# Kernel optimization log

Measured on AMD Instinct MI355X. Metric: run time of the kernel, lower is better.

Reference implementation:

```python
import jax, jax.numpy as jnp
import numpy as np

N, DF, DR, H, K = 4096, 128, 64, 1024, 10


def _init_linear(key, fan_in, fan_out):
    kw, kb = jax.random.split(key)
    bound = 1.0 / np.sqrt(fan_in)
    W = jax.random.uniform(kw, (fan_in, fan_out), jnp.float32, -bound, bound)
    b = jax.random.uniform(kb, (fan_out,), jnp.float32, -bound, bound)
    return W, b


def setup_inputs() -> dict:
    key = jax.random.key(0)
    ks = jax.random.split(key, 8)
    condition = jax.random.normal(ks[0], (N, DF), jnp.float32)
    tensor = jax.random.normal(ks[1], (N, DR), jnp.float32)
    Win, b_in = _init_linear(ks[2], DF + DR, H)
    W1, b1 = _init_linear(ks[3], H, H)
    W2, b2 = _init_linear(ks[4], H, H)
    W3, b3 = _init_linear(ks[5], H, H)
    Wout, b_out = _init_linear(ks[6], H, DR)
    return {"condition": condition, "tensor": tensor,
            "Win": Win, "b_in": b_in, "W1": W1, "b1": b1,
            "W2": W2, "b2": b2, "W3": W3, "b3": b3,
            "Wout": Wout, "b_out": b_out}


def _mlp(x, Win, b_in, W1, b1, W2, b2, W3, b3, Wout, b_out):
    # FFNN: input layer + 3 hidden layers with Softplus, linear output -> DR
    h = jax.nn.softplus(x @ Win + b_in)
    h = jax.nn.softplus(h @ W1 + b1)
    h = jax.nn.softplus(h @ W2 + b2)
    h = jax.nn.softplus(h @ W3 + b3)
    return h @ Wout + b_out


def reference(condition, tensor, Win, b_in, W1, b1, W2, b2, W3, b3, Wout, b_out):
    # torch.cdist(condition, condition), p=2 -> [N, N]
    sq = jnp.sum(condition * condition, axis=-1)
    d2 = sq[:, None] + sq[None, :] - 2.0 * (condition @ condition.T)
    dist = jnp.sqrt(jnp.maximum(d2, 0.0))
    # torch.topk(dist, 10, dim=1, largest=False) -> k nearest neighbor indices
    _, neighbor_idx = jax.lax.top_k(-dist, K)  # [N, K]
    # gather neighbor groups
    cond_g = condition[neighbor_idx]  # [N, K, DF]
    tens_g = tensor[neighbor_idx]     # [N, K, DR]
    # MongeMapNetwork.pushforward: tensor - MLP(concat(condition, tensor))
    x = jnp.concatenate([cond_g, tens_g], axis=-1)  # [N, K, DF+DR]
    pushed = tens_g - _mlp(x, Win, b_in, W1, b1, W2, b2, W3, b3, Wout, b_out)
    return pushed  # [N, K, DR]
```

## Files before the change

kernel.cpp:

```cpp
#include <hip/hip_runtime.h>
#include <hip/hip_fp16.h>
#include <stdint.h>

typedef unsigned short u16;
typedef unsigned int   u32;
typedef unsigned long long u64;
typedef short v8bf __attribute__((ext_vector_type(8)));
typedef float v4f  __attribute__((ext_vector_type(4)));
typedef u16   v8u  __attribute__((ext_vector_type(8)));

#define NPTS 4096
#define DF   128
#define DR   64
#define HID  1024
#define KNN  10
#define DIN  192

#define AS1 __attribute__((address_space(1)))
#define AS3 __attribute__((address_space(3)))

__device__ __forceinline__ float bf2f(u16 b){ return __uint_as_float(((unsigned)b)<<16); }
__device__ __forceinline__ u16 f2bf(float f){
  unsigned u = __float_as_uint(f);
  unsigned r = 0x7fffu + ((u>>16)&1u);
  return (u16)((u + r)>>16);
}
__device__ __forceinline__ u16 f2h(float f){
  __half h = __float2half(f);
  return __half_as_ushort(h);
}
__device__ __forceinline__ float softplus_f(float x){
  return x>15.f ? x : __logf(1.f + __expf(x));
}
__device__ __forceinline__ float rdv(const void* p, long j, int fl){
  return fl ? bf2f(((const u16*)p)[j]) : ((const float*)p)[j];
}
__device__ __forceinline__ void gl2lds16(const u16* g, u16* l){
  __builtin_amdgcn_global_load_lds((const AS1 unsigned int*)g, (AS3 unsigned int*)l, 16, 0, 0);
}

__global__ void detect_k(const u16* __restrict__ c, int* __restrict__ flag){
  __shared__ int cnt[256];
  int t = threadIdx.x, n = 0;
  for(int i=t; i<8192; i+=256){
    u16 v = c[2*i];
    int e = (v>>7)&0xff;
    n += (e>=96 && e<=158);
  }
  cnt[t] = n; __syncthreads();
  for(int s=128; s>0; s>>=1){ if(t<s) cnt[t]+=cnt[t+s]; __syncthreads(); }
  if(t==0) *flag = (cnt[0] > 4915) ? 1 : 0;
}

__global__ void prep_k(const void* cond, const void* tens,
    const void* Wi, const void* W1, const void* W2, const void* W3, const void* Wo,
    const void* bi, const void* b1, const void* b2, const void* b3, const void* bo,
    float* __restrict__ condF, float* __restrict__ tensF, float* __restrict__ biasF,
    u16* Oi, u16* O1, u16* O2, u16* O3, u16* Oo,
    float* __restrict__ sq, u16* __restrict__ X, const int* __restrict__ flag){
  __shared__ u16 tile[32][33];
  const int fl = *flag;
  const int bid = blockIdx.x, tid = threadIdx.x;
  if(bid < 3089){
    int i = bid*256 + tid;
    if(i < 524288){ condF[i] = rdv(cond, i, fl); }
    else if(i < 786432){ tensF[i-524288] = rdv(tens, i-524288, fl); }
    else{
      int j = i - 786432;
      if(j < 1024)      biasF[j] = rdv(bi, j, fl);
      else if(j < 2048) biasF[j] = rdv(b1, j-1024, fl);
      else if(j < 3072) biasF[j] = rdv(b2, j-2048, fl);
      else if(j < 4096) biasF[j] = rdv(b3, j-3072, fl);
      else if(j < 4160) biasF[j] = rdv(bo, j-4096, fl);
    }
  } else if(bid < 6417){
    int b = bid - 3089;
    const void* in; u16* out; int R, C, bx, by;
    if(b < 192)      {              in=Wi; out=Oi; R=192;  C=1024; bx=b&31; by=b>>5; }
    else if(b < 1216){ b -= 192;    in=W1; out=O1; R=1024; C=1024; bx=b&31; by=b>>5; }
    else if(b < 2240){ b -= 1216;   in=W2; out=O2; R=1024; C=1024; bx=b&31; by=b>>5; }
    else if(b < 3264){ b -= 2240;   in=W3; out=O3; R=1024; C=1024; bx=b&31; by=b>>5; }
    else             { b -= 3264;   in=Wo; out=Oo; R=1024; C=64;   bx=b&1;  by=b>>1; }
    int gx = bx*32, gy = by*32;
    int tx = tid&31, ty = tid>>5;
    #pragma unroll
    for(int r=ty; r<32; r+=8){
      size_t idx = (size_t)(gy+r)*C + gx + tx;
      tile[r][tx] = fl ? ((const u16*)in)[idx] : f2bf(((const float*)in)[idx]);
    }
    __syncthreads();
    #pragma unroll
    for(int r=ty; r<32; r+=8) out[(size_t)(gx+r)*R + gy + tx] = tile[tx][r];
  } else if(bid < 7441){
    int b = bid - 6417;
    int row = b*4 + (tid>>6), lane = tid&63;
    float a = rdv(cond, (long)row*DF + lane, fl);
    float c2 = rdv(cond, (long)row*DF + lane + 64, fl);
    double s = (double)a*a + (double)c2*c2;
    #pragma unroll
    for(int off=32; off>0; off>>=1) s += __shfl_down(s, off, 64);
    if(lane==0) sq[row] = (float)s;
  } else {
    int c = (bid-7441)*256 + tid;
    int j = c/48;
    int off = (c - j*48)*4;
    ushort4 o;
    if(off < DF){
      o.x = f2bf(rdv(cond, (long)j*DF + off + 0, fl));
      o.y = f2bf(rdv(cond, (long)j*DF + off + 1, fl));
      o.z = f2bf(rdv(cond, (long)j*DF + off + 2, fl));
      o.w = f2bf(rdv(cond, (long)j*DF + off + 3, fl));
    }else{
      int t2 = off - DF;
      o.x = f2bf(rdv(tens, (long)j*DR + t2 + 0, fl));
      o.y = f2bf(rdv(tens, (long)j*DR + t2 + 1, fl));
      o.z = f2bf(rdv(tens, (long)j*DR + t2 + 2, fl));
      o.w = f2bf(rdv(tens, (long)j*DR + t2 + 3, fl));
    }
    *(ushort4*)&X[(size_t)j*DIN + off] = o;
  }
}

__device__ __forceinline__ void gemm_bt_body(const u16* __restrict__ A,
    const u16* __restrict__ Bt, const float* __restrict__ bias, u16* __restrict__ C,
    int Nc, int Kc, int bid, u16* As, u16* Bs){
  const int xcd = bid&7, slot = bid>>3;
  const int bm = (xcd*4 + (slot>>4)) * 128;
  const int bn = (slot&15) * 64;
  const int tid = threadIdx.x, lane = tid&63, wave = tid>>6;
  const int wm = (wave&1)*64, wn = (wave>>1)*32;
  int c0 = wave*128 + lane, c1 = c0 + 64;
  int r0 = c0>>2, q0 = c0&3, r1 = c1>>2, q1 = c1&3;
  int cb = wave*64 + lane, rb = cb>>2, qb = cb&3;
  const u16* pA0 = A  + (size_t)(bm+r0)*Kc + q0*8;
  const u16* pA1 = A  + (size_t)(bm+r1)*Kc + q1*8;
  const u16* pB  = Bt + (size_t)(bn+rb)*Kc + qb*8;
  u16* lA0 = &As[wave*1024];
  u16* lA1 = &As[wave*1024 + 512];
  u16* lB  = &Bs[wave*512];
  const int m16 = lane&15, q = lane>>4;
  v4f acc[4][2] = {};
  for(int kb=0; kb<Kc; kb+=64){
    gl2lds16(pA0 + kb, lA0);
    gl2lds16(pA1 + kb, lA1);
    gl2lds16(pB  + kb, lB);
    gl2lds16(pA0 + kb + 32, lA0 + 4096);
    gl2lds16(pA1 + kb + 32, lA1 + 4096);
    gl2lds16(pB  + kb + 32, lB + 2048);
    __syncthreads();
    #pragma unroll
    for(int kk=0;kk<2;kk++){
      v8bf a[4], b[2];
      #pragma unroll
      for(int x=0;x<4;x++) a[x] = *(const v8bf*)&As[kk*4096 + (wm + x*16 + m16)*32 + q*8];
      #pragma unroll
      for(int x=0;x<2;x++) b[x] = *(const v8bf*)&Bs[kk*2048 + (wn + x*16 + m16)*32 + q*8];
      #pragma unroll
      for(int mi=0;mi<4;mi++)
        #pragma unroll
        for(int ni=0;ni<2;ni++)
          acc[mi][ni] = __builtin_amdgcn_mfma_f32_16x16x32_bf16(a[mi], b[ni], acc[mi][ni], 0,0,0);
    }
    __syncthreads();
  }
  const int col16 = lane&15, rowq = lane>>4;
  #pragma unroll
  for(int mi=0;mi<4;mi++){
    #pragma unroll
    for(int ni=0;ni<2;ni++){
      int cn = bn + wn + ni*16 + col16;
      float bi = bias[cn];
      #pragma unroll
      for(int r=0;r<4;r++){
        int rw = bm + wm + mi*16 + rowq*4 + r;
        float v = softplus_f(acc[mi][ni][r] + bi);
        C[(size_t)rw*Nc + cn] = f2bf(v);
      }
    }
  }
}

__device__ __forceinline__ void knn_body(const u16* __restrict__ distH,
    const float* __restrict__ condF, int* __restrict__ nidx, int row,
    float* __restrict__ af, int* __restrict__ cand, u64* __restrict__ keys){
  const int lane = threadIdx.x&63;
  af[lane]    = condF[(size_t)row*DF + lane];
  af[lane+64] = condF[(size_t)row*DF + lane + 64];
  const v8u* drow = (const v8u*)(distH + (size_t)row*NPTS);
  v8u vals[8];
  #pragma unroll
  for(int k=0;k<8;k++) vals[k] = drow[lane + k*64];
  u32 mx = 0;
  #pragma unroll
  for(int k=0;k<8;k++)
    #pragma unroll
    for(int e=0;e<8;e++){ u32 v = vals[k][e]; mx = v>mx ? v : mx; }
  #pragma unroll
  for(int off=32; off>0; off>>=1){
    u32 o = (u32)__shfl_down((int)mx, off, 64); mx = o>mx ? o : mx;
  }
  mx = (u32)__shfl((int)mx, 0, 64);
  u32 hi = mx+1, lo = 0;
  for(int it=0; it<17; ++it){
    u32 mid = (lo+hi)>>1;
    int c = 0;
    #pragma unroll
    for(int k=0;k<8;k++)
      #pragma unroll
      for(int e=0;e<8;e++)
        c += (int)__popcll(__ballot((u32)vals[k][e] < mid));
    if(c >= 16){ hi = mid; if(c <= 64) break; }
    else lo = mid;
  }
  const u32 t = hi;
  const u64 below = (1ull<<lane) - 1ull;
  int base = 0;
  #pragma unroll
  for(int k=0;k<8;k++)
    #pragma unroll
    for(int e=0;e<8;e++){
      bool p = (u32)vals[k][e] < t;
      u64 m = __ballot(p);
      if(p){
        int off = base + (int)__popcll(m & below);
        if(off < 64) cand[off] = (lane + k*64)*8 + e;
      }
      base += (int)__popcll(m);
    }
  int cnt = base > 64 ? 64 : base;
  u64 mykey = ~0ULL; int myj = -1;
  if(lane < cnt){
    int j = cand[lane];
    const float4* bp4 = (const float4*)(condF + (size_t)j*DF);
    double s = 0.0;
    #pragma unroll
    for(int v4i=0; v4i<32; v4i++){
      float4 bv = bp4[v4i];
      double d0 = (double)af[v4i*4+0]-(double)bv.x;
      double d1 = (double)af[v4i*4+1]-(double)bv.y;
      double d2 = (double)af[v4i*4+2]-(double)bv.z;
      double d3 = (double)af[v4i*4+3]-(double)bv.w;
      s += d0*d0 + d1*d1 + d2*d2 + d3*d3;
    }
    u64 bits = (u64)__double_as_longlong(s);
    mykey = (bits & ~0xFFFULL) | (u32)j;
    myj = j;
  }
  keys[lane] = mykey;
  if(lane < cnt){
    int rank = 0;
    for(int c2=0;c2<cnt;c2++) rank += (keys[c2] < mykey);
    if(rank < KNN) nidx[row*KNN + rank] = myj;
  }
}

__global__ __launch_bounds__(256,2) void gram_g1_k(const u16* __restrict__ condB,
    const float* __restrict__ condF, const float* __restrict__ sq,
    u16* __restrict__ distH, const int* __restrict__ flag,
    const u16* __restrict__ X, const u16* __restrict__ Wt_in,
    const float* __restrict__ biasF, u16* __restrict__ A0){
  __shared__ __align__(16) u16 smem[20480];
  const int bid = blockIdx.x;
  if(bid < 512){
    gemm_bt_body(X, Wt_in, biasF, A0, HID, DIN, bid, smem, smem+8192);
    return;
  }
  const int gb = bid - 512;
  const int fl = *flag;
  const int bm = (gb&31)*128, bn = (gb>>5)*128;
  const int tid = threadIdx.x, lane = tid&63, wave = tid>>6;
  const int wm = (wave&1)*64, wn = (wave>>1)*64;
  const int m16 = lane&15, q = lane>>4;
  v4f acc[4][4] = {};
  if(fl){
    const int srow = wave*32 + (lane>>2), scol = (lane&3)*8;
    const u16* gA = condB + (size_t)(bm+srow)*DF + scol;
    const u16* gB = condB + (size_t)(bn+srow)*DF + scol;
    u16* lA = &smem[wave*1024];
    u16* lB = &smem[4096 + wave*1024];
    for(int kb=0; kb<DF; kb+=32){
      gl2lds16(gA + kb,                 lA);
      gl2lds16(gA + kb + (size_t)16*DF, lA + 512);
      gl2lds16(gB + kb,                 lB);
      gl2lds16(gB + kb + (size_t)16*DF, lB + 512);
      __syncthreads();
      v8bf a[4], b[4];
      #pragma unroll
      for(int x=0;x<4;x++){
        a[x] = *(const v8bf*)&smem[(wm + x*16 + m16)*32 + q*8];
        b[x] = *(const v8bf*)&smem[4096 + (wn + x*16 + m16)*32 + q*8];
      }
      #pragma unroll
      for(int mi=0;mi<4;mi++)
        #pragma unroll
        for(int ni=0;ni<4;ni++)
          acc[mi][ni] = __builtin_amdgcn_mfma_f32_16x16x32_bf16(a[mi], b[ni], acc[mi][ni], 0,0,0);
      __syncthreads();
    }
  } else {
    u16* Ahi = smem;
    u16* Alo = smem + 5120;
    u16* Bhi = smem + 10240;
    u16* Blo = smem + 15360;
    for(int kb=0; kb<DF; kb+=32){
      #pragma unroll
      for(int t=0;t<4;t++){
        int ch = tid + t*256;
        int r = ch>>3, c = (ch&7)*4;
        float4 av = *(const float4*)&condF[(size_t)(bm+r)*DF + kb + c];
        float4 bv = *(const float4*)&condF[(size_t)(bn+r)*DF + kb + c];
        ushort4 ah, bh, al, bl;
        ah.x=f2bf(av.x); ah.y=f2bf(av.y); ah.z=f2bf(av.z); ah.w=f2bf(av.w);
        bh.x=f2bf(bv.x); bh.y=f2bf(bv.y); bh.z=f2bf(bv.z); bh.w=f2bf(bv.w);
        al.x=f2bf(av.x-bf2f(ah.x)); al.y=f2bf(av.y-bf2f(ah.y));
        al.z=f2bf(av.z-bf2f(ah.z)); al.w=f2bf(av.w-bf2f(ah.w));
        bl.x=f2bf(bv.x-bf2f(bh.x)); bl.y=f2bf(bv.y-bf2f(bh.y));
        bl.z=f2bf(bv.z-bf2f(bh.z)); bl.w=f2bf(bv.w-bf2f(bh.w));
        *(ushort4*)&Ahi[r*40+c] = ah; *(ushort4*)&Bhi[r*40+c] = bh;
        *(ushort4*)&Alo[r*40+c] = al; *(ushort4*)&Blo[r*40+c] = bl;
      }
      __syncthreads();
      v8bf ahf[4], bhf[4], alf[4], blf[4];
      #pragma unroll
      for(int x=0;x<4;x++){
        ahf[x] = *(const v8bf*)&Ahi[(wm + x*16 + m16)*40 + q*8];
        bhf[x] = *(const v8bf*)&Bhi[(wn + x*16 + m16)*40 + q*8];
        alf[x] = *(const v8bf*)&Alo[(wm + x*16 + m16)*40 + q*8];
        blf[x] = *(const v8bf*)&Blo[(wn + x*16 + m16)*40 + q*8];
      }
      #pragma unroll
      for(int mi=0;mi<4;mi++)
        #pragma unroll
        for(int ni=0;ni<4;ni++){
          acc[mi][ni] = __builtin_amdgcn_mfma_f32_16x16x32_bf16(alf[mi], bhf[ni], acc[mi][ni], 0,0,0);
          acc[mi][ni] = __builtin_amdgcn_mfma_f32_16x16x32_bf16(ahf[mi], blf[ni], acc[mi][ni], 0,0,0);
          acc[mi][ni] = __builtin_amdgcn_mfma_f32_16x16x32_bf16(ahf[mi], bhf[ni], acc[mi][ni], 0,0,0);
        }
      __syncthreads();
    }
  }
  const int col16 = lane&15, rowq = lane>>4;
  #pragma unroll
  for(int mi=0;mi<4;mi++){
    #pragma unroll
    for(int ni=0;ni<4;ni++){
      int cj = bn + wn + ni*16 + col16;
      float sqj = sq[cj];
      #pragma unroll
      for(int r=0;r<4;r++){
        int ri = bm + wm + mi*16 + rowq*4 + r;
        float d2 = (sq[ri] + sqj) - 2.0f*acc[mi][ni][r];
        distH[(size_t)ri*NPTS + cj] = f2h(fmaxf(d2, 0.f));
      }
    }
  }
}

__global__ __launch_bounds__(256,2) void gemm_knn_k(const u16* __restrict__ A,
    const u16* __restrict__ Bt, const float* __restrict__ bias, u16* __restrict__ C,
    const u16* __restrict__ distH, const float* __restrict__ condF,
    int* __restrict__ nidx, int rowoff){
  __shared__ __align__(16) u16 gsm[12288];
  __shared__ float af[4][DF];
  __shared__ int   cand[4][64];
  __shared__ u64   keys[4][64];
  const int bid = blockIdx.x;
  if(bid < 512){
    gemm_bt_body(A, Bt, bias, C, HID, HID, bid, gsm, gsm+8192);
  } else {
    const int wv = threadIdx.x>>6;
    const int row = rowoff + (bid-512)*4 + wv;
    knn_body(distH, condF, nidx, row, af[wv], cand[wv], keys[wv]);
  }
}

__global__ __launch_bounds__(256,2) void gemm_bt_k(const u16* __restrict__ A,
    const u16* __restrict__ Bt, const float* __restrict__ bias, u16* __restrict__ C){
  __shared__ __align__(16) u16 As[8192];
  __shared__ __align__(16) u16 Bs[4096];
  gemm_bt_body(A, Bt, bias, C, HID, HID, blockIdx.x, As, Bs);
}

__global__ __launch_bounds__(256,2) void gemm_out_k(const u16* __restrict__ A,
    const u16* __restrict__ Bt, float* __restrict__ Pp){
  __shared__ __align__(16) u16 As[128*32];
  __shared__ __align__(16) u16 Bs[64*32];
  const int bm = (blockIdx.x>>2)*128;
  const int k0 = (blockIdx.x&3)*256;
  float* P = Pp + (size_t)(blockIdx.x&3)*262144;
  const int tid = threadIdx.x, lane = tid&63, wave = tid>>6;
  const int wm = wave*32;
  int c0 = wave*128 + lane, c1 = c0 + 64;
  int ra0 = c0>>2, qa0 = c0&3, ra1 = c1>>2, qa1 = c1&3;
  int cb = wave*64 + lane;
  int rb = cb>>2, qb = cb&3;
  const u16* pA0 = A  + (size_t)(bm+ra0)*HID + qa0*8;
  const u16* pA1 = A  + (size_t)(bm+ra1)*HID + qa1*8;
  const u16* pB  = Bt + (size_t)rb*HID + qb*8;
  u16* lA0 = &As[(wave*128     )*8];
  u16* lA1 = &As[(wave*128 + 64)*8];
  u16* lB  = &Bs[(wave*64      )*8];
  const int m16 = lane&15, q = lane>>4;
  v4f acc[2][4] = {};
  for(int kb=k0; kb<k0+256; kb+=32){
    gl2lds16(pA0 + kb, lA0);
    gl2lds16(pA1 + kb, lA1);
    gl2lds16(pB  + kb, lB);
    __syncthreads();
    v8bf a[2], b[4];
    a[0] = *(const v8bf*)&As[(wm + m16)*32 + q*8];
    a[1] = *(const v8bf*)&As[(wm + 16 + m16)*32 + q*8];
    #pragma unroll
    for(int x=0;x<4;x++) b[x] = *(const v8bf*)&Bs[(x*16 + m16)*32 + q*8];
    #pragma unroll
    for(int mi=0;mi<2;mi++)
      #pragma unroll
      for(int ni=0;ni<4;ni++)
        acc[mi][ni] = __builtin_amdgcn_mfma_f32_16x16x32_bf16(a[mi], b[ni], acc[mi][ni], 0,0,0);
    __syncthreads();
  }
  const int col16 = lane&15, rowq = lane>>4;
  #pragma unroll
  for(int mi=0;mi<2;mi++){
    #pragma unroll
    for(int ni=0;ni<4;ni++){
      int cn = ni*16 + col16;
      #pragma unroll
      for(int r=0;r<4;r++){
        int rw = bm + wm + mi*16 + rowq*4 + r;
        P[(size_t)rw*DR + cn] = acc[mi][ni][r];
      }
    }
  }
}

__global__ void gather_k(const float* __restrict__ Pp, const float* __restrict__ tensF,
                         const float* __restrict__ biasF, const int* __restrict__ nidx,
                         void* __restrict__ outv, const int* __restrict__ flag){
  const int fl = *flag;
  int e = blockIdx.x*256 + threadIdx.x;
  int m = e>>4;
  int c = (e&15)*4;
  int j = nidx[m] & (NPTS-1);
  size_t rc = (size_t)j*DR + c;
  float4 t  = *(const float4*)&tensF[rc];
  float4 b  = *(const float4*)&biasF[4096 + c];
  float4 p0 = *(const float4*)&Pp[rc];
  float4 p1 = *(const float4*)&Pp[262144 + rc];
  float4 p2 = *(const float4*)&Pp[524288 + rc];
  float4 p3 = *(const float4*)&Pp[786432 + rc];
  float4 v;
  v.x = t.x - (b.x + ((p0.x+p1.x)+(p2.x+p3.x)));
  v.y = t.y - (b.y + ((p0.y+p1.y)+(p2.y+p3.y)));
  v.z = t.z - (b.z + ((p0.z+p1.z)+(p2.z+p3.z)));
  v.w = t.w - (b.w + ((p0.w+p1.w)+(p2.w+p3.w)));
  if(fl){
    ushort4 o; o.x=f2bf(v.x); o.y=f2bf(v.y); o.z=f2bf(v.z); o.w=f2bf(v.w);
    *(ushort4*)&((u16*)outv)[(size_t)m*DR + c] = o;
  }else{
    *(float4*)&((float*)outv)[(size_t)m*DR + c] = v;
  }
}

constexpr size_t OFF_FLAG  = 0;
constexpr size_t OFF_SQ    = 256;
constexpr size_t OFF_NIDX  = OFF_SQ    + 16384;
constexpr size_t OFF_BIAS  = OFF_NIDX  + 163840;
constexpr size_t OFF_CONDF = OFF_BIAS  + 16640;
constexpr size_t OFF_TENSF = OFF_CONDF + 2097152;
constexpr size_t OFF_WTIN  = OFF_TENSF + 1048576;
constexpr size_t OFF_WT1   = OFF_WTIN  + 393216;
constexpr size_t OFF_WT2   = OFF_WT1   + 2097152;
constexpr size_t OFF_WT3   = OFF_WT2   + 2097152;
constexpr size_t OFF_WTO   = OFF_WT3   + 2097152;
constexpr size_t OFF_DIST  = OFF_WTO   + 131072;
constexpr size_t OFF_X     = OFF_DIST  + 33554432;
constexpr size_t OFF_A0    = OFF_X     + 1572864;
constexpr size_t OFF_A1    = OFF_A0    + 8388608;
constexpr size_t OFF_P     = OFF_A1    + 8388608;

extern "C" void kernel_launch(void* const* d_in, const int* in_sizes, int n_in,
                              void* d_out, int out_size, void* d_ws, size_t ws_size,
                              hipStream_t stream){
  char* ws = (char*)d_ws;
  int*   flag  = (int*)  (ws + OFF_FLAG);
  float* sqv   = (float*)(ws + OFF_SQ);
  int*   nidx  = (int*)  (ws + OFF_NIDX);
  float* biasF = (float*)(ws + OFF_BIAS);
  float* condF = (float*)(ws + OFF_CONDF);
  float* tensF = (float*)(ws + OFF_TENSF);
  u16*   Wt_in = (u16*)  (ws + OFF_WTIN);
  u16*   Wt1   = (u16*)  (ws + OFF_WT1);
  u16*   Wt2   = (u16*)  (ws + OFF_WT2);
  u16*   Wt3   = (u16*)  (ws + OFF_WT3);
  u16*   Wt_o  = (u16*)  (ws + OFF_WTO);
  u16*   distH = (u16*)  (ws + OFF_DIST);
  u16*   X     = (u16*)  (ws + OFF_X);
  u16*   A0    = (u16*)  (ws + OFF_A0);
  u16*   A1    = (u16*)  (ws + OFF_A1);
  float* Pp    = (float*)(ws + OFF_P);

  detect_k <<<1, 256, 0, stream>>>((const u16*)d_in[0], flag);
  prep_k   <<<8209, 256, 0, stream>>>(d_in[0], d_in[1],
                d_in[2], d_in[4], d_in[6], d_in[8], d_in[10],
                d_in[3], d_in[5], d_in[7], d_in[9], d_in[11],
                condF, tensF, biasF, Wt_in, Wt1, Wt2, Wt3, Wt_o, sqv, X, flag);
  gram_g1_k<<<1536, 256, 0, stream>>>((const u16*)d_in[0], condF, sqv, distH, flag,
                                      X, Wt_in, biasF, A0);
  gemm_knn_k<<<1024, 256, 0, stream>>>(A0, Wt1, biasF+1024, A1, distH, condF, nidx, 0);
  gemm_knn_k<<<1024, 256, 0, stream>>>(A1, Wt2, biasF+2048, A0, distH, condF, nidx, 2048);
  gemm_bt_k  <<<512, 256, 0, stream>>>(A0, Wt3, biasF+3072, A1);
  gemm_out_k <<<128, 256, 0, stream>>>(A1, Wt_o, Pp);
  gather_k   <<<2560, 256, 0, stream>>>(Pp, tensF, biasF, nidx, d_out, flag);
}
```

Before: 210.5 us.

## Fuse all stages into a persistent megakernel with software grid barriers

Replaces the eight separate kernel launches with a single persistent kernel of 512 blocks. The stages (prep, input GEMM plus Gram, hidden GEMMs overlapped with KNN, output GEMM, gather) are separated by atomic-counter grid barriers. Each block runs flag detection itself, and the hidden GEMMs are reassigned to 256 blocks doing two tiles each while the other blocks do KNN. The goal is to remove launch gaps and tail effects between stages, at the cost of spin-wait barriers, less parallelism within each stage, and reliance on all 512 blocks being co-resident (checked through an occupancy query).

```diff
diff --git a/kernel.cpp b/kernel.cpp
--- a/kernel.cpp
+++ b/kernel.cpp
@@ -15,6 +15,7 @@
 #define HID  1024
 #define KNN  10
 #define DIN  192
+#define NB   512
 
 #define AS1 __attribute__((address_space(1)))
 #define AS3 __attribute__((address_space(3)))
@@ -39,30 +40,65 @@
   __builtin_amdgcn_global_load_lds((const AS1 unsigned int*)g, (AS3 unsigned int*)l, 16, 0, 0);
 }
 
-__global__ void detect_k(const u16* __restrict__ c, int* __restrict__ flag){
-  __shared__ int cnt[256];
-  int t = threadIdx.x, n = 0;
-  for(int i=t; i<8192; i+=256){
+constexpr size_t OFF_BAR   = 0;
+constexpr size_t OFF_FLAG  = 128;
+constexpr size_t OFF_SQ    = 256;
+constexpr size_t OFF_NIDX  = OFF_SQ    + 16384;
+constexpr size_t OFF_BIAS  = OFF_NIDX  + 163840;
+constexpr size_t OFF_CONDF = OFF_BIAS  + 16640;
+constexpr size_t OFF_TENSF = OFF_CONDF + 2097152;
+constexpr size_t OFF_WTIN  = OFF_TENSF + 1048576;
+constexpr size_t OFF_WT1   = OFF_WTIN  + 393216;
+constexpr size_t OFF_WT2   = OFF_WT1   + 2097152;
+constexpr size_t OFF_WT3   = OFF_WT2   + 2097152;
+constexpr size_t OFF_WTO   = OFF_WT3   + 2097152;
+constexpr size_t OFF_DIST  = OFF_WTO   + 131072;
+constexpr size_t OFF_X     = OFF_DIST  + 33554432;
+constexpr size_t OFF_A0    = OFF_X     + 1572864;
+constexpr size_t OFF_A1    = OFF_A0    + 8388608;
+constexpr size_t OFF_P     = OFF_A1    + 8388608;
+
+__device__ __forceinline__ void gbar(u32* cnt, u32* rel, u32 e){
+  __syncthreads();
+  if(threadIdx.x == 0){
+    __threadfence();
+    u32 a = __hip_atomic_fetch_add(cnt, 1u, __ATOMIC_ACQ_REL, __HIP_MEMORY_SCOPE_AGENT);
+    if(a == e*NB + (NB-1)){
+      __hip_atomic_store(rel, e+1u, __ATOMIC_RELEASE, __HIP_MEMORY_SCOPE_AGENT);
+    } else {
+      while(__hip_atomic_load(rel, __ATOMIC_ACQUIRE, __HIP_MEMORY_SCOPE_AGENT) <= e)
+        __builtin_amdgcn_s_sleep(2);
+    }
+    __threadfence();
+  }
+  __syncthreads();
+}
+
+__device__ __forceinline__ int detect_fl(const void* cond, u16* SM){
+  const u16* c = (const u16*)cond;
+  int tid = threadIdx.x, n = 0;
+  for(int i=tid; i<8192; i+=256){
     u16 v = c[2*i];
     int e = (v>>7)&0xff;
     n += (e>=96 && e<=158);
   }
-  cnt[t] = n; __syncthreads();
-  for(int s=128; s>0; s>>=1){ if(t<s) cnt[t]+=cnt[t+s]; __syncthreads(); }
-  if(t==0) *flag = (cnt[0] > 4915) ? 1 : 0;
-}
-
-__global__ void prep_k(const void* cond, const void* tens,
+  int* cnt = (int*)SM;
+  cnt[tid] = n; __syncthreads();
+  for(int s=128; s>0; s>>=1){ if(tid<s) cnt[tid]+=cnt[tid+s]; __syncthreads(); }
+  int fl = (cnt[0] > 4915) ? 1 : 0;
+  __syncthreads();
+  return fl;
+}
+
+__device__ __forceinline__ void prep_unit(int u, int tid, int fl,
+    const void* cond, const void* tens,
     const void* Wi, const void* W1, const void* W2, const void* W3, const void* Wo,
     const void* bi, const void* b1, const void* b2, const void* b3, const void* bo,
-    float* __restrict__ condF, float* __restrict__ tensF, float* __restrict__ biasF,
+    float* condF, float* tensF, float* biasF,
     u16* Oi, u16* O1, u16* O2, u16* O3, u16* Oo,
-    float* __restrict__ sq, u16* __restrict__ X, const int* __restrict__ flag){
-  __shared__ u16 tile[32][33];
-  const int fl = *flag;
-  const int bid = blockIdx.x, tid = threadIdx.x;
-  if(bid < 3089){
-    int i = bid*256 + tid;
+    float* sq, u16* X, u16* SM){
+  if(u < 3089){
+    int i = u*256 + tid;
     if(i < 524288){ condF[i] = rdv(cond, i, fl); }
     else if(i < 786432){ tensF[i-524288] = rdv(tens, i-524288, fl); }
     else{
@@ -73,8 +109,9 @@
       else if(j < 4096) biasF[j] = rdv(b3, j-3072, fl);
       else if(j < 4160) biasF[j] = rdv(bo, j-4096, fl);
     }
-  } else if(bid < 6417){
-    int b = bid - 3089;
+  } else if(u < 6417){
+    u16 (*tile)[33] = (u16(*)[33])SM;
+    int b = u - 3089;
     const void* in; u16* out; int R, C, bx, by;
     if(b < 192)      {              in=Wi; out=Oi; R=192;  C=1024; bx=b&31; by=b>>5; }
     else if(b < 1216){ b -= 192;    in=W1; out=O1; R=1024; C=1024; bx=b&31; by=b>>5; }
@@ -91,8 +128,8 @@
     __syncthreads();
     #pragma unroll
     for(int r=ty; r<32; r+=8) out[(size_t)(gx+r)*R + gy + tx] = tile[tx][r];
-  } else if(bid < 7441){
-    int b = bid - 6417;
+  } else if(u < 7441){
+    int b = u - 6417;
     int row = b*4 + (tid>>6), lane = tid&63;
     float a = rdv(cond, (long)row*DF + lane, fl);
     float c2 = rdv(cond, (long)row*DF + lane + 64, fl);
@@ -101,7 +138,7 @@
     for(int off=32; off>0; off>>=1) s += __shfl_down(s, off, 64);
     if(lane==0) sq[row] = (float)s;
   } else {
-    int c = (bid-7441)*256 + tid;
+    int c = (u-7441)*256 + tid;
     int j = c/48;
     int off = (c - j*48)*4;
     ushort4 o;
@@ -254,19 +291,9 @@
   }
 }
 
-__global__ __launch_bounds__(256,2) void gram_g1_k(const u16* __restrict__ condB,
-    const float* __restrict__ condF, const float* __restrict__ sq,
-    u16* __restrict__ distH, const int* __restrict__ flag,
-    const u16* __restrict__ X, const u16* __restrict__ Wt_in,
-    const float* __restrict__ biasF, u16* __restrict__ A0){
-  __shared__ __align__(16) u16 smem[20480];
-  const int bid = blockIdx.x;
-  if(bid < 512){
-    gemm_bt_body(X, Wt_in, biasF, A0, HID, DIN, bid, smem, smem+8192);
-    return;
-  }
-  const int gb = bid - 512;
-  const int fl = *flag;
+__device__ __forceinline__ void gram_tile(int gb, int fl,
+    const u16* __restrict__ condB, const float* __restrict__ condF,
+    const float* __restrict__ sq, u16* __restrict__ distH, u16* SM){
   const int bm = (gb&31)*128, bn = (gb>>5)*128;
   const int tid = threadIdx.x, lane = tid&63, wave = tid>>6;
   const int wm = (wave&1)*64, wn = (wave>>1)*64;
@@ -276,8 +303,8 @@
     const int srow = wave*32 + (lane>>2), scol = (lane&3)*8;
     const u16* gA = condB + (size_t)(bm+srow)*DF + scol;
     const u16* gB = condB + (size_t)(bn+srow)*DF + scol;
-    u16* lA = &smem[wave*1024];
-    u16* lB = &smem[4096 + wave*1024];
+    u16* lA = &SM[wave*1024];
+    u16* lB = &SM[4096 + wave*1024];
     for(int kb=0; kb<DF; kb+=32){
       gl2lds16(gA + kb,                 lA);
       gl2lds16(gA + kb + (size_t)16*DF, lA + 512);
@@ -287,8 +314,8 @@
       v8bf a[4], b[4];
       #pragma unroll
       for(int x=0;x<4;x++){
-        a[x] = *(const v8bf*)&smem[(wm + x*16 + m16)*32 + q*8];
-        b[x] = *(const v8bf*)&smem[4096 + (wn + x*16 + m16)*32 + q*8];
+        a[x] = *(const v8bf*)&SM[(wm + x*16 + m16)*32 + q*8];
+        b[x] = *(const v8bf*)&SM[4096 + (wn + x*16 + m16)*32 + q*8];
       }
       #pragma unroll
       for(int mi=0;mi<4;mi++)
@@ -298,10 +325,10 @@
       __syncthreads();
     }
   } else {
-    u16* Ahi = smem;
-    u16* Alo = smem + 5120;
-    u16* Bhi = smem + 10240;
-    u16* Blo = smem + 15360;
+    u16* Ahi = SM;
+    u16* Alo = SM + 5120;
+    u16* Bhi = SM + 10240;
+    u16* Blo = SM + 15360;
     for(int kb=0; kb<DF; kb+=32){
       #pragma unroll
       for(int t=0;t<4;t++){
@@ -356,38 +383,11 @@
   }
 }
 
-__global__ __launch_bounds__(256,2) void gemm_knn_k(const u16* __restrict__ A,
-    const u16* __restrict__ Bt, const float* __restrict__ bias, u16* __restrict__ C,
-    const u16* __restrict__ distH, const float* __restrict__ condF,
-    int* __restrict__ nidx, int rowoff){
-  __shared__ __align__(16) u16 gsm[12288];
-  __shared__ float af[4][DF];
-  __shared__ int   cand[4][64];
-  __shared__ u64   keys[4][64];
-  const int bid = blockIdx.x;
-  if(bid < 512){
-    gemm_bt_body(A, Bt, bias, C, HID, HID, bid, gsm, gsm+8192);
-  } else {
-    const int wv = threadIdx.x>>6;
-    const int row = rowoff + (bid-512)*4 + wv;
-    knn_body(distH, condF, nidx, row, af[wv], cand[wv], keys[wv]);
-  }
-}
-
-__global__ __launch_bounds__(256,2) void gemm_bt_k(const u16* __restrict__ A,
-    const u16* __restrict__ Bt, const float* __restrict__ bias, u16* __restrict__ C){
-  __shared__ __align__(16) u16 As[8192];
-  __shared__ __align__(16) u16 Bs[4096];
-  gemm_bt_body(A, Bt, bias, C, HID, HID, blockIdx.x, As, Bs);
-}
-
-__global__ __launch_bounds__(256,2) void gemm_out_k(const u16* __restrict__ A,
-    const u16* __restrict__ Bt, float* __restrict__ Pp){
-  __shared__ __align__(16) u16 As[128*32];
-  __shared__ __align__(16) u16 Bs[64*32];
-  const int bm = (blockIdx.x>>2)*128;
-  const int k0 = (blockIdx.x&3)*256;
-  float* P = Pp + (size_t)(blockIdx.x&3)*262144;
+__device__ __forceinline__ void gemm_out_body(int obid, const u16* __restrict__ A,
+    const u16* __restrict__ Bt, float* __restrict__ Pp, u16* As, u16* Bs){
+  const int bm = (obid>>2)*128;
+  const int k0 = (obid&3)*256;
+  float* P = Pp + (size_t)(obid&3)*262144;
   const int tid = threadIdx.x, lane = tid&63, wave = tid>>6;
   const int wm = wave*32;
   int c0 = wave*128 + lane, c1 = c0 + 64;
@@ -434,11 +434,9 @@
   }
 }
 
-__global__ void gather_k(const float* __restrict__ Pp, const float* __restrict__ tensF,
-                         const float* __restrict__ biasF, const int* __restrict__ nidx,
-                         void* __restrict__ outv, const int* __restrict__ flag){
-  const int fl = *flag;
-  int e = blockIdx.x*256 + threadIdx.x;
+__device__ __forceinline__ void gather_unit(int e, int fl,
+    const float* Pp, const float* tensF, const float* biasF,
+    const int* nidx, void* outv){
   int m = e>>4;
   int c = (e&15)*4;
   int j = nidx[m] & (NPTS-1);
@@ -462,22 +460,166 @@
   }
 }
 
-constexpr size_t OFF_FLAG  = 0;
-constexpr size_t OFF_SQ    = 256;
-constexpr size_t OFF_NIDX  = OFF_SQ    + 16384;
-constexpr size_t OFF_BIAS  = OFF_NIDX  + 163840;
-constexpr size_t OFF_CONDF = OFF_BIAS  + 16640;
-constexpr size_t OFF_TENSF = OFF_CONDF + 2097152;
-constexpr size_t OFF_WTIN  = OFF_TENSF + 1048576;
-constexpr size_t OFF_WT1   = OFF_WTIN  + 393216;
-constexpr size_t OFF_WT2   = OFF_WT1   + 2097152;
-constexpr size_t OFF_WT3   = OFF_WT2   + 2097152;
-constexpr size_t OFF_WTO   = OFF_WT3   + 2097152;
-constexpr size_t OFF_DIST  = OFF_WTO   + 131072;
-constexpr size_t OFF_X     = OFF_DIST  + 33554432;
-constexpr size_t OFF_A0    = OFF_X     + 1572864;
-constexpr size_t OFF_A1    = OFF_A0    + 8388608;
-constexpr size_t OFF_P     = OFF_A1    + 8388608;
+__global__ void __launch_bounds__(256,2) mega_k(
+    const void* cond, const void* tens,
+    const void* Wi, const void* W1w, const void* W2w, const void* W3w, const void* Wow,
+    const void* bi, const void* b1, const void* b2, const void* b3, const void* bo,
+    char* ws, void* outv){
+  __shared__ __align__(16) u16 SM[20480];
+  const int bid = blockIdx.x, tid = threadIdx.x;
+
+  u32*   bcnt  = (u32*)  (ws + OFF_BAR);
+  u32*   brel  = (u32*)  (ws + OFF_BAR + 8);
+  float* sqv   = (float*)(ws + OFF_SQ);
+  int*   nidx  = (int*)  (ws + OFF_NIDX);
+  float* biasF = (float*)(ws + OFF_BIAS);
+  float* condF = (float*)(ws + OFF_CONDF);
+  float* tensF = (float*)(ws + OFF_TENSF);
+  u16*   Wt_in = (u16*)  (ws + OFF_WTIN);
+  u16*   Wt1   = (u16*)  (ws + OFF_WT1);
+  u16*   Wt2   = (u16*)  (ws + OFF_WT2);
+  u16*   Wt3   = (u16*)  (ws + OFF_WT3);
+  u16*   Wt_o  = (u16*)  (ws + OFF_WTO);
+  u16*   distH = (u16*)  (ws + OFF_DIST);
+  u16*   X     = (u16*)  (ws + OFF_X);
+  u16*   A0    = (u16*)  (ws + OFF_A0);
+  u16*   A1    = (u16*)  (ws + OFF_A1);
+  float* Pp    = (float*)(ws + OFF_P);
+
+  const int fl = detect_fl(cond, SM);
+
+  for(int u=bid; u<8209; u+=NB){
+    prep_unit(u, tid, fl, cond, tens, Wi, W1w, W2w, W3w, Wow, bi, b1, b2, b3, bo,
+              condF, tensF, biasF, Wt_in, Wt1, Wt2, Wt3, Wt_o, sqv, X, SM);
+    __syncthreads();
+  }
+  gbar(bcnt, brel, 0);
+
+  gemm_bt_body(X, Wt_in, biasF, A0, HID, DIN, bid, SM, SM+8192);
+  __syncthreads();
+  for(int gb=bid; gb<1024; gb+=NB){
+    gram_tile(gb, fl, (const u16*)cond, condF, sqv, distH, SM);
+    __syncthreads();
+  }
+  gbar(bcnt, brel, 1);
+
+  const int wv = tid>>6;
+  float* kaf  = (float*)SM + wv*128;
+  int*   kcan = (int*)((char*)SM + 2048) + wv*64;
+  u64*   kkey = (u64*)((char*)SM + 4096) + wv*64;
+
+  if(bid < 256){
+    gemm_bt_body(A0, Wt1, biasF+1024, A1, HID, HID, bid,     SM, SM+8192);
+    __syncthreads();
+    gemm_bt_body(A0, Wt1, biasF+1024, A1, HID, HID, bid+256, SM, SM+8192);
+  } else {
+    knn_body(distH, condF, nidx, (bid-256)*4 + wv, kaf, kcan, kkey);
+  }
+  gbar(bcnt, brel, 2);
+
+  if(bid < 256){
+    gemm_bt_body(A1, Wt2, biasF+2048, A0, HID, HID, bid,     SM, SM+8192);
+    __syncthreads();
+    gemm_bt_body(A1, Wt2, biasF+2048, A0, HID, HID, bid+256, SM, SM+8192);
+  } else {
+    knn_body(distH, condF, nidx, 1024 + (bid-256)*4 + wv, kaf, kcan, kkey);
+  }
+  gbar(bcnt, brel, 3);
+
+  if(bid < 256){
+    gemm_bt_body(A0, Wt3, biasF+3072, A1, HID, HID, bid,     SM, SM+8192);
+    __syncthreads();
+    gemm_bt_body(A0, Wt3, biasF+3072, A1, HID, HID, bid+256, SM, SM+8192);
+  } else {
+    knn_body(distH, condF, nidx, 2048 + (bid-256)*4 + wv, kaf, kcan, kkey);
+  }
+  gbar(bcnt, brel, 4);
+
+  if(bid < 128){
+    gemm_out_body(bid, A1, Wt_o, Pp, SM, SM+8192);
+  } else if(bid >= 256){
+    knn_body(distH, condF, nidx, 3072 + (bid-256)*4 + wv, kaf, kcan, kkey);
+  }
+  gbar(bcnt, brel, 5);
+
+  for(int u=bid; u<2560; u+=NB)
+    gather_unit(u*256 + tid, fl, Pp, tensF, biasF, nidx, outv);
+}
+
+__global__ void detect_k(const u16* __restrict__ c, int* __restrict__ flag){
+  __shared__ int cnt[256];
+  int t = threadIdx.x, n = 0;
+  for(int i=t; i<8192; i+=256){
+    u16 v = c[2*i];
+    int e = (v>>7)&0xff;
+    n += (e>=96 && e<=158);
+  }
+  cnt[t] = n; __syncthreads();
+  for(int s=128; s>0; s>>=1){ if(t<s) cnt[t]+=cnt[t+s]; __syncthreads(); }
+  if(t==0) *flag = (cnt[0] > 4915) ? 1 : 0;
+}
+
+__global__ void prep_k(const void* cond, const void* tens,
+    const void* Wi, const void* W1, const void* W2, const void* W3, const void* Wo,
+    const void* bi, const void* b1, const void* b2, const void* b3, const void* bo,
+    float* condF, float* tensF, float* biasF,
+    u16* Oi, u16* O1, u16* O2, u16* O3, u16* Oo,
+    float* sq, u16* X, const int* __restrict__ flag){
+  __shared__ __align__(16) u16 SM[1056];
+  prep_unit(blockIdx.x, threadIdx.x, *flag, cond, tens, Wi, W1, W2, W3, Wo,
+            bi, b1, b2, b3, bo, condF, tensF, biasF, Oi, O1, O2, O3, Oo, sq, X, SM);
+}
+
+__global__ __launch_bounds__(256,2) void gram_g1_k(const u16* __restrict__ condB,
+    const float* __restrict__ condF, const float* __restrict__ sq,
+    u16* __restrict__ distH, const int* __restrict__ flag,
+    const u16* __restrict__ X, const u16* __restrict__ Wt_in,
+    const float* __restrict__ biasF, u16* __restrict__ A0){
+  __shared__ __align__(16) u16 SM[20480];
+  const int bid = blockIdx.x;
+  if(bid < 512){
+    gemm_bt_body(X, Wt_in, biasF, A0, HID, DIN, bid, SM, SM+8192);
+  } else {
+    gram_tile(bid-512, *flag, condB, condF, sq, distH, SM);
+  }
+}
+
+__global__ __launch_bounds__(256,2) void gemm_knn_k(const u16* __restrict__ A,
+    const u16* __restrict__ Bt, const float* __restrict__ bias, u16* __restrict__ C,
+    const u16* __restrict__ distH, const float* __restrict__ condF,
+    int* __restrict__ nidx, int rowoff){
+  __shared__ __align__(16) u16 gsm[12288];
+  __shared__ float af[4][DF];
+  __shared__ int   cand[4][64];
+  __shared__ u64   keys[4][64];
+  const int bid = blockIdx.x;
+  if(bid < 512){
+    gemm_bt_body(A, Bt, bias, C, HID, HID, bid, gsm, gsm+8192);
+  } else {
+    const int wv = threadIdx.x>>6;
+    knn_body(distH, condF, nidx, rowoff + (bid-512)*4 + wv, af[wv], cand[wv], keys[wv]);
+  }
+}
+
+__global__ __launch_bounds__(256,2) void gemm_bt_k(const u16* __restrict__ A,
+    const u16* __restrict__ Bt, const float* __restrict__ bias, u16* __restrict__ C){
+  __shared__ __align__(16) u16 As[8192];
+  __shared__ __align__(16) u16 Bs[4096];
+  gemm_bt_body(A, Bt, bias, C, HID, HID, blockIdx.x, As, Bs);
+}
+
+__global__ __launch_bounds__(256,2) void gemm_out_k(const u16* __restrict__ A,
+    const u16* __restrict__ Bt, float* __restrict__ Pp){
+  __shared__ __align__(16) u16 As[4096];
+  __shared__ __align__(16) u16 Bs[2048];
+  gemm_out_body(blockIdx.x, A, Bt, Pp, As, Bs);
+}
+
+__global__ void gather_k(const float* __restrict__ Pp, const float* __restrict__ tensF,
+                         const float* __restrict__ biasF, const int* __restrict__ nidx,
+                         void* __restrict__ outv, const int* __restrict__ flag){
+  gather_unit(blockIdx.x*256 + threadIdx.x, *flag, Pp, tensF, biasF, nidx, outv);
+}
 
 extern "C" void kernel_launch(void* const* d_in, const int* in_sizes, int n_in,
                               void* d_out, int out_size, void* d_ws, size_t ws_size,
@@ -500,6 +642,22 @@
   u16*   A1    = (u16*)  (ws + OFF_A1);
   float* Pp    = (float*)(ws + OFF_P);
 
+  static int occ_cached = -1;
+  if(occ_cached < 0){
+    int occ = 0;
+    if(hipOccupancyMaxActiveBlocksPerMultiprocessor(&occ, (const void*)mega_k, 256, 0)
+       != hipSuccess) occ = 0;
+    occ_cached = occ;
+  }
+
+  if(occ_cached >= 2){
+    hipMemsetAsync(ws + OFF_BAR, 0, 64, stream);
+    hipLaunchKernelGGL(mega_k, dim3(NB), dim3(256), 0, stream,
+        d_in[0], d_in[1], d_in[2], d_in[4], d_in[6], d_in[8], d_in[10],
+        d_in[3], d_in[5], d_in[7], d_in[9], d_in[11], ws, d_out);
+    return;
+  }
+
   detect_k <<<1, 256, 0, stream>>>((const u16*)d_in[0], flag);
   prep_k   <<<8209, 256, 0, stream>>>(d_in[0], d_in[1],
                 d_in[2], d_in[4], d_in[6], d_in[8], d_in[10],
```

Result: no change. 206.6 us (-1.9%).
